# Kernel tuning notes

Hardware: AMD Instinct MI355X
Metric: run time of the kernel (lower is better)

## Reference

```python
import jax, jax.numpy as jnp
import numpy as np

# ---- constants matching init_kwargs ----
N_SAMPLES = 64
NEAR, FAR = 0.1, 8.0
N_AZI, N_ELE = 32, 16
SPEED = 343.0
FS = 16000.0
PATHLOSS = 1.0
XYZ_MIN = jnp.array([-5.0, -5.0, -3.0], dtype=jnp.float32)
XYZ_MAX = jnp.array([5.0, 5.0, 3.0], dtype=jnp.float32)
L = 512  # n_lenseq
HID = 64


def _normalize(p):
    return 2.0 * (p - XYZ_MIN) / (XYZ_MAX - XYZ_MIN) - 1.0


def _denormalize(p):
    return (p + 1.0) / 2.0 * (XYZ_MAX - XYZ_MIN) + XYZ_MIN


def _ray_directions():
    key = jax.random.key(42)
    azi = jnp.linspace(0.0, 2.0 * jnp.pi, N_AZI + 1)[:-1]
    azi = azi + (2.0 * jnp.pi / N_AZI) * jax.random.uniform(key, (N_AZI,))
    ele = jnp.linspace(0.0, 1.0, N_ELE + 2)[1:-1]  # random add multiplied by 0 in source
    ele = jnp.arccos(2.0 * ele - 1.0)
    a, e = jnp.meshgrid(azi, ele, indexing='ij')
    a, e = a.ravel(), e.ravel()
    d = jnp.stack([jnp.cos(a) * jnp.sin(e), jnp.sin(a) * jnp.sin(e), jnp.cos(e)], axis=1)
    poles = jnp.array([[0.0, 0.0, 1.0], [0.0, 0.0, -1.0]], dtype=d.dtype)
    return jnp.concatenate([d, poles], axis=0)  # [R, 3], R = N_AZI*N_ELE + 2


def setup_inputs() -> dict:
    key = jax.random.key(0)
    ks = jax.random.split(key, 7)
    return {
        'rays_o': jax.random.uniform(ks[0], (2, 3), minval=-4.0, maxval=4.0, dtype=jnp.float32),
        'position_tx': jax.random.uniform(ks[1], (2, 3), minval=-4.0, maxval=4.0, dtype=jnp.float32),
        'W1': jax.random.normal(ks[2], (9, HID), dtype=jnp.float32) * 0.3,
        'b1': jax.random.normal(ks[3], (HID,), dtype=jnp.float32) * 0.1,
        'w_attn': jax.random.normal(ks[4], (HID,), dtype=jnp.float32) * 0.3,
        'W_sig': jax.random.normal(ks[5], (HID, L), dtype=jnp.float32) * 0.1,
        'b_sig': jax.random.normal(ks[6], (L,), dtype=jnp.float32) * 0.01,
    }


def reference(rays_o, position_tx, W1, b1, w_attn, W_sig, b_sig):
    bs = position_tx.shape[0]
    dirs = _ray_directions()                          # [R, 3]
    R = dirs.shape[0]
    d_vals = jnp.linspace(0.0, 1.0, N_SAMPLES) * (FAR - NEAR) + NEAR  # [S]

    # ray points: [bs, R, S, 3]
    ray_pts = rays_o[:, None, None, :] + dirs[None, :, None, :] * d_vals[None, None, :, None]
    network_pts = _normalize(ray_pts.reshape(bs, -1, 3))              # [bs, N, 3]
    network_view = jnp.broadcast_to(-dirs[None, :, None, :], ray_pts.shape).reshape(bs, -1, 3)
    network_tx = jnp.broadcast_to(_normalize(position_tx)[:, None, :], network_pts.shape)

    # inline MLP replacing network_fn
    feats = jnp.concatenate([network_pts, network_view, network_tx], axis=-1)  # [bs, N, 9]
    h = jax.nn.relu(jnp.einsum('bnf,fh->bnh', feats, W1) + b1)
    attn = jax.nn.softplus(jnp.einsum('bnh,h->bn', h, w_attn)).reshape(bs, R, N_SAMPLES)
    signal = (jnp.einsum('bnh,hl->bnl', h, W_sig) + b_sig).reshape(bs, R, N_SAMPLES, L)

    # tail mask (receiver delay)
    pts2rx_idx = FS * d_vals / SPEED                  # [S]
    shift_samples = jnp.round(pts2rx_idx)             # [S]
    rev = jnp.arange(L - 1, -1, -1)
    mask_tail = (rev[None, :].astype(jnp.float32) - shift_samples[:, None] > 0).astype(signal.dtype)  # [S, L]
    signal = signal * mask_tail

    # tx->point delay mask
    tx2pts_idx = jnp.linalg.norm(_denormalize(network_tx - network_pts), axis=-1).reshape(bs, R, N_SAMPLES) * FS / SPEED
    delay = jnp.clip(jnp.round(tx2pts_idx), 0, L - 1)[..., None]      # [bs, R, S, 1]
    mask_tx = (jnp.arange(L)[None, None, None, :] >= delay).astype(signal.dtype)
    signal = signal * mask_tx

    # path loss gather (vectorized replacement of the python loop + cpu sync)
    prev_part = int(0.1 / SPEED * FS)
    ideal = jnp.arange(0, int(L * 2.5)).astype(jnp.float32) / FS * SPEED
    path_loss = PATHLOSS / (ideal + 0.001)
    path_loss = path_loss.at[:prev_part].set(path_loss[prev_part + 1])
    idx = shift_samples.astype(jnp.int32)[:, None] + jnp.arange(L)[None, :]  # [S, L]
    path_loss_all = path_loss[idx]                                          # [S, L]

    # fractional delay via phase shift in frequency domain
    fft_sig = jnp.fft.rfft(signal * path_loss_all, axis=-1)                 # [bs, R, S, F]
    F = L // 2 + 1
    phase = jnp.exp(-1j * 2.0 * jnp.pi / L * jnp.arange(F)[None, :] * pts2rx_idx[:, None])  # [S, F]
    shifted = fft_sig * phase

    # acoustic volume rendering
    dists = jnp.concatenate([d_vals[1:] - d_vals[:-1], jnp.array([1e10], dtype=d_vals.dtype)])  # [S]
    alpha = 1.0 - jnp.exp(-attn * dists)                                    # [bs, R, S]
    ones = jnp.ones(alpha[..., :1].shape, dtype=alpha.dtype)
    att_i = jnp.cumprod(jnp.concatenate([ones, 1.0 - alpha + 1e-6], axis=-1), axis=-1)[..., :-1]
    n_rays_signal = jnp.sum(shifted * (att_i * alpha)[..., None], axis=-2)  # [bs, R, F]

    receive = jnp.sum(n_rays_signal, axis=-2)                               # [bs, F]
    return jnp.stack([jnp.real(receive), jnp.imag(receive)], axis=-1)       # [bs, F, 2]
```

## Files before the change

kernel.cpp:

```cpp
#include <hip/hip_runtime.h>
#include <hip/hip_fp16.h>
#include <stdint.h>
#include <math.h>

#define BS    2
#define RAYS  514
#define NS    64
#define LSEQ  512
#define NF    257
#define HIDN  64
#define SPLIT 4
#define JC    16

#define TWO_PI_F 6.28318530717958647692f

__device__ __forceinline__ uint32_t rotl32(uint32_t x, int d){ return (x<<d)|(x>>(32-d)); }

__device__ __forceinline__ void tf_rounds4(uint32_t& x0, uint32_t& x1, int a, int b, int c, int d){
  x0+=x1; x1=rotl32(x1,a); x1^=x0;
  x0+=x1; x1=rotl32(x1,b); x1^=x0;
  x0+=x1; x1=rotl32(x1,c); x1^=x0;
  x0+=x1; x1=rotl32(x1,d); x1^=x0;
}

__device__ void threefry2x32(uint32_t k0, uint32_t k1, uint32_t x0, uint32_t x1,
                             uint32_t& o0, uint32_t& o1)
{
  const uint32_t ks2 = k0 ^ k1 ^ 0x1BD11BDAu;
  x0 += k0; x1 += k1;
  tf_rounds4(x0,x1,13,15,26,6);   x0+=k1;  x1+=ks2+1u;
  tf_rounds4(x0,x1,17,29,16,24);  x0+=ks2; x1+=k0+2u;
  tf_rounds4(x0,x1,13,15,26,6);   x0+=k0;  x1+=k1+3u;
  tf_rounds4(x0,x1,17,29,16,24);  x0+=k1;  x1+=ks2+4u;
  tf_rounds4(x0,x1,13,15,26,6);   x0+=ks2; x1+=k0+5u;
  o0 = x0; o1 = x1;
}

__device__ void ray_dir(int r, float d[3])
{
  if (r >= 512) { d[0]=0.f; d[1]=0.f; d[2] = (r==512) ? 1.0f : -1.0f; return; }
  int i = r >> 4, j = r & 15;
  uint32_t o0, o1;
  threefry2x32(0u, 42u, 0u, (uint32_t)i, o0, o1);
  uint32_t bits = o0 ^ o1;
  float u = __uint_as_float((bits >> 9) | 0x3F800000u) - 1.0f;
  const float step = TWO_PI_F / 32.0f;
  float a = (float)i * step + step * u;
  float e = acosf(2.0f * ((float)(j+1) * (1.0f/17.0f)) - 1.0f);
  float se = sinf(e);
  d[0] = cosf(a) * se;
  d[1] = sinf(a) * se;
  d[2] = cosf(e);
}

__device__ __forceinline__ float dval(int s){ return ((float)s*(1.0f/63.0f))*7.9f + 0.1f; }

__device__ __forceinline__ uint32_t pk2(float a, float b){
  return (uint32_t)__half_as_ushort(__float2half(a)) |
         ((uint32_t)__half_as_ushort(__float2half(b)) << 16);
}

__global__ __launch_bounds__(256)
void k1_rays(const float* __restrict__ rays_o, const float* __restrict__ position_tx,
             const float* __restrict__ W1, const float* __restrict__ b1,
             const float* __restrict__ w_attn,
             __half* __restrict__ wh, float* __restrict__ w_arr, int* __restrict__ delay_arr,
             float* __restrict__ g, float* __restrict__ out)
{
  const int tid = threadIdx.x;
  const int wid = tid >> 6, lane = tid & 63;
  const int br = blockIdx.x*4 + wid;
  const int b = br / RAYS, r = br % RAYS;

  {
    int gi = blockIdx.x*256 + tid;
    if (gi < BS*NS*LSEQ) g[gi] = 0.f;
    if (gi < BS*NF*2) out[gi] = 0.f;
  }

  float dir[3]; ray_dir(r, dir);
  const float mn[3] = {-5.f,-5.f,-3.f}, mx[3] = {5.f,5.f,3.f};
  float ro[3], ntx[3];
  #pragma unroll
  for (int c=0;c<3;c++){
    ro[c] = rays_o[b*3+c];
    float t = position_tx[b*3+c];
    ntx[c] = 2.0f*(t - mn[c])/(mx[c]-mn[c]) - 1.0f;
  }

  const float dv = dval(lane);
  float feat[9], dd2 = 0.f;
  #pragma unroll
  for (int c=0;c<3;c++){
    float pt = ro[c] + dir[c]*dv;
    float npt = 2.0f*(pt - mn[c])/(mx[c]-mn[c]) - 1.0f;
    float ddc = ((ntx[c]-npt) + 1.0f)/2.0f*(mx[c]-mn[c]) + mn[c];
    dd2 += ddc*ddc;
    feat[c]   = npt;
    feat[3+c] = -dir[c];
    feat[6+c] = ntx[c];
  }

  float h[HIDN];
  float av = 0.f;
  #pragma unroll
  for (int j=0; j<HIDN; j++){
    float hj = b1[j];
    #pragma unroll
    for (int f=0; f<9; f++) hj = fmaf(feat[f], W1[f*HIDN + j], hj);
    hj = fmaxf(hj, 0.0f);
    h[j] = hj;
    av = fmaf(hj, w_attn[j], av);
  }

  float attn = fmaxf(av, 0.f) + log1pf(expf(-fabsf(av)));
  float dist = (lane < NS-1) ? (dval(lane+1) - dv) : 1e10f;
  float alpha = 1.0f - expf(-attn*dist);

  float fac = 1.0f - alpha + 1e-6f;
  float scan = fac;
  #pragma unroll
  for (int m=1; m<64; m<<=1){
    float up = __shfl_up(scan, m, 64);
    if (lane >= m) scan *= up;
  }
  float T = __shfl_up(scan, 1, 64);
  if (lane == 0) T = 1.0f;
  float wgt = T * alpha;

  float delf = fminf(fmaxf(rintf(sqrtf(dd2)*16000.0f/343.0f), 0.f), 511.f);

  const int bsid = b*NS + lane;
  const int o2 = bsid*RAYS + r;
  w_arr[o2] = wgt;
  delay_arr[o2] = (int)delf;

  #pragma unroll
  for (int p=0; p<SPLIT; p++){
    uint4 v0, v1;
    v0.x = pk2(wgt*h[p*16+ 0], wgt*h[p*16+ 1]);
    v0.y = pk2(wgt*h[p*16+ 2], wgt*h[p*16+ 3]);
    v0.z = pk2(wgt*h[p*16+ 4], wgt*h[p*16+ 5]);
    v0.w = pk2(wgt*h[p*16+ 6], wgt*h[p*16+ 7]);
    v1.x = pk2(wgt*h[p*16+ 8], wgt*h[p*16+ 9]);
    v1.y = pk2(wgt*h[p*16+10], wgt*h[p*16+11]);
    v1.z = pk2(wgt*h[p*16+12], wgt*h[p*16+13]);
    v1.w = pk2(wgt*h[p*16+14], wgt*h[p*16+15]);
    uint4* dst = (uint4*)(wh + (((size_t)p*BS*NS + bsid)*RAYS + r)*16);
    dst[0] = v0; dst[1] = v1;
  }
}

__global__ __launch_bounds__(512)
void k2_bucket(const __half* __restrict__ wh, const float* __restrict__ w_arr,
               const int* __restrict__ delay_arr,
               const float* __restrict__ W_sig, const float* __restrict__ b_sig,
               float* __restrict__ g)
{
  __shared__ __align__(16) ushort sorted_h[RAYS*16];
  __shared__ float  sorted_w[RAYS];
  __shared__ float  P[RAYS][JC+1];
  __shared__ float  part[32][JC+1];
  __shared__ int    hist[LSEQ];
  __shared__ int    cum[LSEQ];
  __shared__ int    delay_l[RAYS];
  __shared__ float  w_l[RAYS];
  __shared__ int    wtot[8];

  const int blk = blockIdx.x;
  const int bsid = blk / SPLIT, p = blk % SPLIT;
  const int tid = threadIdx.x;
  const int wv = tid >> 6, lane = tid & 63;
  const int obase = bsid * RAYS;
  int* posbuf = (int*)&part[0][0];

  hist[tid] = 0;
  for (int i = tid; i < RAYS; i += 512){
    delay_l[i] = delay_arr[obase + i];
    if (p == 0) w_l[i] = w_arr[obase + i];
  }
  __syncthreads();

  for (int i = tid; i < RAYS; i += 512) atomicAdd(&hist[delay_l[i]], 1);
  __syncthreads();

  int h0 = hist[tid];
  {
    int v = h0;
    #pragma unroll
    for (int m=1; m<64; m<<=1){ int u = __shfl_up(v, m, 64); if (lane >= m) v += u; }
    if (lane == 63) wtot[wv] = v;
    __syncthreads();
    int off = 0;
    for (int t=0; t<wv; t++) off += wtot[t];
    int cumv = v + off;
    cum[tid] = cumv;
    hist[tid] = cumv - h0;
  }
  __syncthreads();

  for (int i = tid; i < RAYS; i += 512)
    posbuf[i] = atomicAdd(&hist[delay_l[i]], 1);
  __syncthreads();

  {
    const uint4* whp = (const uint4*)(wh + ((size_t)p*BS*NS + bsid)*RAYS*16);
    uint4* s4 = (uint4*)sorted_h;
    for (int idx = tid; idx < RAYS*2; idx += 512){
      int r = idx >> 1, half = idx & 1;
      uint4 v = whp[idx];
      s4[posbuf[r]*2 + half] = v;
    }
    if (p == 0)
      for (int i = tid; i < RAYS; i += 512) sorted_w[posbuf[i]] = w_l[i];
  }
  __syncthreads();

  const int seg = tid >> 4, col = tid & 15;
  const int r0 = seg*17;
  const int re = max(0, min(17, RAYS - r0));
  {
    float run = 0.f;
    for (int k=0; k<re; k++){
      run += __half2float(__ushort_as_half(sorted_h[(r0+k)*16 + col]));
      P[r0+k][col] = run;
    }
    part[seg][col] = run;
    if (p == 0 && col == 15){
      float rw = 0.f;
      for (int k=0; k<re; k++){ rw += sorted_w[r0+k]; P[r0+k][JC] = rw; }
      part[seg][JC] = rw;
    }
  }
  __syncthreads();

  if (lane < 32){
    float v1 = part[lane][wv], v2 = part[lane][wv+8];
    #pragma unroll
    for (int m=1; m<32; m<<=1){
      float u1 = __shfl_up(v1, m, 32);
      float u2 = __shfl_up(v2, m, 32);
      if (lane >= m){ v1 += u1; v2 += u2; }
    }
    part[lane][wv] = v1; part[lane][wv+8] = v2;
    if (wv == 7 && p == 0){
      float vw = part[lane][JC];
      #pragma unroll
      for (int m=1; m<32; m<<=1){
        float uw = __shfl_up(vw, m, 32);
        if (lane >= m) vw += uw;
      }
      part[lane][JC] = vw;
    }
  }
  __syncthreads();

  {
    float off = (seg > 0) ? part[seg-1][col] : 0.f;
    for (int k=0; k<re; k++) P[r0+k][col] += off;
    if (p == 0 && col == 15){
      float ow = (seg > 0) ? part[seg-1][JC] : 0.f;
      for (int k=0; k<re; k++) P[r0+k][JC] += ow;
    }
  }
  __syncthreads();

  const int s = bsid % NS;
  const float dv = dval(s);
  const float shiftf = rintf((16000.0f*dv)/343.0f);
  const int shift = (int)shiftf;
  const int jbase = p*JC;
  {
    const int l = tid;
    float mt = (((float)(LSEQ-1-l)) - shiftf > 0.f) ? 1.f : 0.f;
    const int c = cum[l];
    if (mt > 0.f && c > 0){
      const int row = c - 1;
      float acc = 0.f;
      #pragma unroll
      for (int jj=0;jj<JC;jj++) acc += P[row][jj] * W_sig[(jbase+jj)*LSEQ + l];
      if (p == 0) acc += b_sig[l] * P[row][JC];
      int pli = shift + l;
      if (pli < 4) pli = 5;
      float ideal = ((float)pli/16000.0f)*343.0f;
      atomicAdd(&g[bsid*LSEQ + l], acc / (ideal + 0.001f));
    }
  }
}

__global__ __launch_bounds__(256)
void k3_dft(const float* __restrict__ g, float* __restrict__ out)
{
  __shared__ float4 gs4[LSEQ/4];
  __shared__ float red[4][64][2];
  const int blk = blockIdx.x;
  const int bsid = blk >> 2, grp = blk & 3;
  const int b = bsid / NS, s = bsid % NS;
  const int tid = threadIdx.x;
  const int c = tid >> 6, bl = tid & 63;

  if (tid < LSEQ/4) gs4[tid] = ((const float4*)(g + bsid*LSEQ))[tid];
  __syncthreads();

  const int k = grp*64 + bl;
  float re = 0.f, im = 0.f;
  {
    float s1, c1; sincosf(-(TWO_PI_F/512.0f)*(float)k, &s1, &c1);
    float c2 = c1*c1 - s1*s1,  s2 = 2.0f*c1*s1;
    float c3 = c1*c2 - s1*s2,  s3 = c1*s2 + s1*c2;
    float c4 = c2*c2 - s2*s2,  s4 = 2.0f*c2*s2;
    const int l0 = c*128;
    int t0 = (k*l0) & (LSEQ-1);
    float wi, wr; sincosf(-(TWO_PI_F/512.0f)*(float)t0, &wi, &wr);
    for (int q=0; q<32; q++){
      float4 gv = gs4[c*32 + q];
      float pr = gv.x + gv.y*c1 + gv.z*c2 + gv.w*c3;
      float pi =        gv.y*s1 + gv.z*s2 + gv.w*s3;
      re = fmaf(pr, wr, re); re = fmaf(-pi, wi, re);
      im = fmaf(pr, wi, im); im = fmaf( pi, wr, im);
      float nr = wr*c4 - wi*s4;
      wi = fmaf(wr, s4, wi*c4);
      wr = nr;
    }
  }
  red[c][bl][0] = re; red[c][bl][1] = im;
  __syncthreads();

  const float cfrac = (16000.0f*dval(s))/343.0f;
  if (tid < 64){
    const int kk = grp*64 + tid;
    float rs = red[0][tid][0] + red[1][tid][0] + red[2][tid][0] + red[3][tid][0];
    float is = red[0][tid][1] + red[1][tid][1] + red[2][tid][1] + red[3][tid][1];
    float ang = -(TWO_PI_F/512.0f)*((float)kk*cfrac);
    float sp, cp; sincosf(ang, &sp, &cp);
    atomicAdd(&out[(b*NF + kk)*2],     rs*cp - is*sp);
    atomicAdd(&out[(b*NF + kk)*2 + 1], rs*sp + is*cp);
  } else if (grp == 0 && tid < 128){
    int t = tid - 64;
    float4 a = gs4[t], bq = gs4[t+64];
    float alt = (a.x - a.y + a.z - a.w) + (bq.x - bq.y + bq.z - bq.w);
    #pragma unroll
    for (int m=32; m>=1; m>>=1) alt += __shfl_xor(alt, m, 64);
    if (t == 0){
      float ang = -(TWO_PI_F/512.0f)*(256.0f*cfrac);
      float sp, cp; sincosf(ang, &sp, &cp);
      atomicAdd(&out[(b*NF + 256)*2],     alt*cp);
      atomicAdd(&out[(b*NF + 256)*2 + 1], alt*sp);
    }
  }
}

extern "C" void kernel_launch(void* const* d_in, const int* in_sizes, int n_in,
                              void* d_out, int out_size, void* d_ws, size_t ws_size,
                              hipStream_t stream)
{
  const float* rays_o      = (const float*)d_in[0];
  const float* position_tx = (const float*)d_in[1];
  const float* W1          = (const float*)d_in[2];
  const float* b1          = (const float*)d_in[3];
  const float* w_attn      = (const float*)d_in[4];
  const float* W_sig       = (const float*)d_in[5];
  const float* b_sig       = (const float*)d_in[6];
  float* out = (float*)d_out;

  char* ws = (char*)d_ws;
  __half* wh       = (__half*)ws;
  float* w_arr     = (float*)(ws + 8421376);
  int*   delay_arr = (int*)  (ws + 8421376 + 263168);
  float* g         = (float*)(ws + 8421376 + 2*263168);

  k1_rays  <<<(BS*RAYS)/4,  256, 0, stream>>>(rays_o, position_tx, W1, b1, w_attn,
                                              wh, w_arr, delay_arr, g, out);
  k2_bucket<<<BS*NS*SPLIT,  512, 0, stream>>>(wh, w_arr, delay_arr, W_sig, b_sig, g);
  k3_dft   <<<BS*NS*4,      256, 0, stream>>>(g, out);
}
```

Measured before the change: 34.46 us.

## Fuse bucket accumulation and DFT into one kernel, dropping intermediate buffer

The DFT stage moves into the tail of the bucket kernel. Each block takes its partial time-domain signal (one hidden-dim split) from shared memory, runs a full 257-bin DFT on it and atomically adds the phase-shifted result into the output. This relies on the DFT being linear across the split partials. It removes the third launch, the zeroing of the global intermediate buffer and its global atomics. In exchange, total DFT work grows by the split factor (4), each block runs a longer serial loop over 512 samples, and more blocks contend on the same output atomics.

```diff
diff --git a/kernel.cpp b/kernel.cpp
--- a/kernel.cpp
+++ b/kernel.cpp
@@ -65,7 +65,7 @@
              const float* __restrict__ W1, const float* __restrict__ b1,
              const float* __restrict__ w_attn,
              __half* __restrict__ wh, float* __restrict__ w_arr, int* __restrict__ delay_arr,
-             float* __restrict__ g, float* __restrict__ out)
+             float* __restrict__ out)
 {
   const int tid = threadIdx.x;
   const int wid = tid >> 6, lane = tid & 63;
@@ -74,7 +74,6 @@
 
   {
     int gi = blockIdx.x*256 + tid;
-    if (gi < BS*NS*LSEQ) g[gi] = 0.f;
     if (gi < BS*NF*2) out[gi] = 0.f;
   }
 
@@ -152,10 +151,10 @@
 }
 
 __global__ __launch_bounds__(512)
-void k2_bucket(const __half* __restrict__ wh, const float* __restrict__ w_arr,
-               const int* __restrict__ delay_arr,
-               const float* __restrict__ W_sig, const float* __restrict__ b_sig,
-               float* __restrict__ g)
+void k2_fused(const __half* __restrict__ wh, const float* __restrict__ w_arr,
+              const int* __restrict__ delay_arr,
+              const float* __restrict__ W_sig, const float* __restrict__ b_sig,
+              float* __restrict__ out)
 {
   __shared__ __align__(16) ushort sorted_h[RAYS*16];
   __shared__ float  sorted_w[RAYS];
@@ -166,6 +165,7 @@
   __shared__ int    delay_l[RAYS];
   __shared__ float  w_l[RAYS];
   __shared__ int    wtot[8];
+  __shared__ __align__(16) float gs[LSEQ];
 
   const int blk = blockIdx.x;
   const int bsid = blk / SPLIT, p = blk % SPLIT;
@@ -268,12 +268,13 @@
   const int s = bsid % NS;
   const float dv = dval(s);
   const float shiftf = rintf((16000.0f*dv)/343.0f);
-  const int shift = (int)shiftf;
-  const int jbase = p*JC;
-  {
+  {
+    const int shift = (int)shiftf;
+    const int jbase = p*JC;
     const int l = tid;
     float mt = (((float)(LSEQ-1-l)) - shiftf > 0.f) ? 1.f : 0.f;
     const int c = cum[l];
+    float val = 0.f;
     if (mt > 0.f && c > 0){
       const int row = c - 1;
       float acc = 0.f;
@@ -283,60 +284,43 @@
       int pli = shift + l;
       if (pli < 4) pli = 5;
       float ideal = ((float)pli/16000.0f)*343.0f;
-      atomicAdd(&g[bsid*LSEQ + l], acc / (ideal + 0.001f));
-    }
-  }
-}
-
-__global__ __launch_bounds__(256)
-void k3_dft(const float* __restrict__ g, float* __restrict__ out)
-{
-  __shared__ float4 gs4[LSEQ/4];
-  __shared__ float red[4][64][2];
-  const int blk = blockIdx.x;
-  const int bsid = blk >> 2, grp = blk & 3;
-  const int b = bsid / NS, s = bsid % NS;
-  const int tid = threadIdx.x;
-  const int c = tid >> 6, bl = tid & 63;
-
-  if (tid < LSEQ/4) gs4[tid] = ((const float4*)(g + bsid*LSEQ))[tid];
-  __syncthreads();
-
-  const int k = grp*64 + bl;
-  float re = 0.f, im = 0.f;
-  {
+      val = acc / (ideal + 0.001f);
+    }
+    gs[l] = val;
+  }
+  __syncthreads();
+
+  const float4* gs4 = (const float4*)gs;
+  const int b = bsid / NS;
+  const float cfrac = (16000.0f*dv)/343.0f;
+  if (tid < 256){
+    const int k = tid;
     float s1, c1; sincosf(-(TWO_PI_F/512.0f)*(float)k, &s1, &c1);
     float c2 = c1*c1 - s1*s1,  s2 = 2.0f*c1*s1;
     float c3 = c1*c2 - s1*s2,  s3 = c1*s2 + s1*c2;
     float c4 = c2*c2 - s2*s2,  s4 = 2.0f*c2*s2;
-    const int l0 = c*128;
-    int t0 = (k*l0) & (LSEQ-1);
-    float wi, wr; sincosf(-(TWO_PI_F/512.0f)*(float)t0, &wi, &wr);
-    for (int q=0; q<32; q++){
-      float4 gv = gs4[c*32 + q];
-      float pr = gv.x + gv.y*c1 + gv.z*c2 + gv.w*c3;
-      float pi =        gv.y*s1 + gv.z*s2 + gv.w*s3;
-      re = fmaf(pr, wr, re); re = fmaf(-pi, wi, re);
-      im = fmaf(pr, wi, im); im = fmaf( pi, wr, im);
-      float nr = wr*c4 - wi*s4;
-      wi = fmaf(wr, s4, wi*c4);
-      wr = nr;
-    }
-  }
-  red[c][bl][0] = re; red[c][bl][1] = im;
-  __syncthreads();
-
-  const float cfrac = (16000.0f*dval(s))/343.0f;
-  if (tid < 64){
-    const int kk = grp*64 + tid;
-    float rs = red[0][tid][0] + red[1][tid][0] + red[2][tid][0] + red[3][tid][0];
-    float is = red[0][tid][1] + red[1][tid][1] + red[2][tid][1] + red[3][tid][1];
-    float ang = -(TWO_PI_F/512.0f)*((float)kk*cfrac);
+    float re = 0.f, im = 0.f;
+    #pragma unroll
+    for (int chunk=0; chunk<4; chunk++){
+      int t0 = (k*(chunk*128)) & (LSEQ-1);
+      float wi, wr; sincosf(-(TWO_PI_F/512.0f)*(float)t0, &wi, &wr);
+      for (int q=0; q<32; q++){
+        float4 gv = gs4[chunk*32 + q];
+        float pr = gv.x + gv.y*c1 + gv.z*c2 + gv.w*c3;
+        float pi =        gv.y*s1 + gv.z*s2 + gv.w*s3;
+        re = fmaf(pr, wr, re); re = fmaf(-pi, wi, re);
+        im = fmaf(pr, wi, im); im = fmaf( pi, wr, im);
+        float nr = wr*c4 - wi*s4;
+        wi = fmaf(wr, s4, wi*c4);
+        wr = nr;
+      }
+    }
+    float ang = -(TWO_PI_F/512.0f)*((float)k*cfrac);
     float sp, cp; sincosf(ang, &sp, &cp);
-    atomicAdd(&out[(b*NF + kk)*2],     rs*cp - is*sp);
-    atomicAdd(&out[(b*NF + kk)*2 + 1], rs*sp + is*cp);
-  } else if (grp == 0 && tid < 128){
-    int t = tid - 64;
+    atomicAdd(&out[(b*NF + k)*2],     re*cp - im*sp);
+    atomicAdd(&out[(b*NF + k)*2 + 1], re*sp + im*cp);
+  } else if (tid < 320){
+    int t = tid - 256;
     float4 a = gs4[t], bq = gs4[t+64];
     float alt = (a.x - a.y + a.z - a.w) + (bq.x - bq.y + bq.z - bq.w);
     #pragma unroll
@@ -367,10 +351,8 @@
   __half* wh       = (__half*)ws;
   float* w_arr     = (float*)(ws + 8421376);
   int*   delay_arr = (int*)  (ws + 8421376 + 263168);
-  float* g         = (float*)(ws + 8421376 + 2*263168);
-
-  k1_rays  <<<(BS*RAYS)/4,  256, 0, stream>>>(rays_o, position_tx, W1, b1, w_attn,
-                                              wh, w_arr, delay_arr, g, out);
-  k2_bucket<<<BS*NS*SPLIT,  512, 0, stream>>>(wh, w_arr, delay_arr, W_sig, b_sig, g);
-  k3_dft   <<<BS*NS*4,      256, 0, stream>>>(g, out);
-}
+
+  k1_rays <<<(BS*RAYS)/4, 256, 0, stream>>>(rays_o, position_tx, W1, b1, w_attn,
+                                            wh, w_arr, delay_arr, out);
+  k2_fused<<<BS*NS*SPLIT, 512, 0, stream>>>(wh, w_arr, delay_arr, W_sig, b_sig, out);
+}
```

After: 112.3 us. 226% more time.
